# Performance work log

Hardware: AMD Instinct MI355X
Metric: run time of the kernel (lower is better)

Reference implementation:

```python
import math
import jax, jax.numpy as jnp
import numpy as np

B, N, M, C, H = 64, 64, 64, 512, 8
HD = C // H
FREQ = 256  # frequency_embedding_size
MAX_PERIOD = 10000.0


def setup_inputs() -> dict:
    key = jax.random.key(0)
    ks = jax.random.split(key, 10)
    s = 1.0 / math.sqrt(C)
    sf = 1.0 / math.sqrt(FREQ)
    return {
        "query": jax.random.normal(ks[0], (B, N, C), jnp.float32),
        "query_pos": jax.random.uniform(ks[1], (1, N, M), jnp.float32),
        # projection weights stored as [in, out]
        "Wq": jax.random.normal(ks[2], (C, C), jnp.float32) * s,
        "bq": jnp.zeros((C,), jnp.float32),
        "Wk": jax.random.normal(ks[3], (C, C), jnp.float32) * s,  # no bias
        "Wv": jax.random.normal(ks[4], (C, C), jnp.float32) * s,
        "bv": jnp.zeros((C,), jnp.float32),
        "Wo": jax.random.normal(ks[5], (C, C), jnp.float32) * s,
        "bo": jnp.zeros((C,), jnp.float32),
        # ScalarEmbedder MLP: Linear(FREQ->C), SiLU, Linear(C->C)
        "W1": jax.random.normal(ks[6], (FREQ, C), jnp.float32) * sf,
        "b1": jnp.zeros((C,), jnp.float32),
        "W2": jax.random.normal(ks[7], (C, C), jnp.float32) * s,
        "b2": jnp.zeros((C,), jnp.float32),
    }


def _freqs():
    half = FREQ // 2
    return jnp.exp(-math.log(MAX_PERIOD) * jnp.arange(half, dtype=jnp.float32) / half)


def reference(query, query_pos, Wq, bq, Wk, Wv, bv, Wo, bo, W1, b1, W2, b2):
    Bq, Nq, Cq = query.shape
    Mk = query_pos.shape[-1]
    # --- ScalarEmbedder on flattened pairwise positions: [N*M] -> [N*M, C]
    t = query_pos.reshape(-1)                       # [Bp*N*M], Bp = 1
    tf = t[:, None] * _freqs()[None, :]             # [N*M, FREQ/2]
    emb = jnp.concatenate([jnp.cos(tf), jnp.sin(tf)], axis=-1)  # [N*M, FREQ]
    pe = jax.nn.silu(emb @ W1 + b1) @ W2 + b2        # [N*M, C]
    pe = pe.reshape(Nq, Mk, H, HD).transpose(2, 0, 1, 3)  # [H, N, M, hd] (tiled over B via broadcast)

    q = (query @ Wq + bq).reshape(Bq, Nq, H, HD)     # bnhd
    k = (query @ Wk).reshape(Bq, Mk, H, HD)          # bmhd (key = query)
    v = (query @ Wv + bv).reshape(Bq, Mk, H, HD)

    scale = HD ** -0.5
    # attn[b,h,n,m] = sum_d q[b,n,h,d] * pe[h,n,m,d] * k[b,m,h,d]
    scores = jnp.einsum("bnhd,hnmd,bmhd->bhnm", q, pe, k) * scale
    attn = jax.nn.softmax(scores, axis=-1)
    x = jnp.einsum("bhnm,bmhd->bnhd", attn, v).reshape(Bq, Nq, Cq)
    return x @ Wo + bo + query  # identity = query
```

## Files before the change

kernel.cpp:

```cpp
#include <hip/hip_runtime.h>
#include <hip/hip_bf16.h>
#include <math.h>

typedef short short8 __attribute__((ext_vector_type(8)));
typedef float floatx4 __attribute__((ext_vector_type(4)));

__device__ __forceinline__ ushort f2bf(float f) {
    __hip_bfloat16 h = __float2bfloat16(f);
    return *reinterpret_cast<ushort*>(&h);
}
__device__ __forceinline__ void bf8_to_f32(uint4 u, float* f) {
    f[0] = __uint_as_float(u.x << 16); f[1] = __uint_as_float(u.x & 0xffff0000u);
    f[2] = __uint_as_float(u.y << 16); f[3] = __uint_as_float(u.y & 0xffff0000u);
    f[4] = __uint_as_float(u.z << 16); f[5] = __uint_as_float(u.z & 0xffff0000u);
    f[6] = __uint_as_float(u.w << 16); f[7] = __uint_as_float(u.w & 0xffff0000u);
}

#define GLDS16(g, l) __builtin_amdgcn_global_load_lds( \
    (const __attribute__((address_space(1))) void*)(g), \
    (__attribute__((address_space(3))) void*)(l), 16, 0, 0)

__global__ __launch_bounds__(256) void prep_kernel(
        const float* __restrict__ W1, const float* __restrict__ W2,
        const float* __restrict__ Wq, const float* __restrict__ Wk,
        const float* __restrict__ Wv, const float* __restrict__ Wo,
        const float* __restrict__ bq, const float* __restrict__ bv,
        const float* __restrict__ query, const float* __restrict__ qpos,
        ushort* __restrict__ W1t, ushort* __restrict__ W2t,
        ushort* __restrict__ Wqkvt, ushort* __restrict__ Wot,
        ushort* __restrict__ queryB, ushort* __restrict__ embB,
        float* __restrict__ biasC) {
    const int z = blockIdx.z;
    const int tx = threadIdx.x, ty = threadIdx.y;
    const int tid = ty * 32 + tx;
    if (z < 6) {
        const float* src; ushort* dst; int R;
        switch (z) {
            case 0:  src = W1; dst = W1t;              R = 256; break;
            case 1:  src = W2; dst = W2t;              R = 512; break;
            case 2:  src = Wq; dst = Wqkvt;            R = 512; break;
            case 3:  src = Wk; dst = Wqkvt + 512*512;  R = 512; break;
            case 4:  src = Wv; dst = Wqkvt + 1024*512; R = 512; break;
            default: src = Wo; dst = Wot;              R = 512; break;
        }
        const int r0 = blockIdx.y * 32, c0 = blockIdx.x * 32;
        if (r0 >= R) return;
        __shared__ float t[32][33];
        for (int i = ty; i < 32; i += 8) t[i][tx] = src[(size_t)(r0 + i) * 512 + c0 + tx];
        __syncthreads();
        for (int i = ty; i < 32; i += 8) dst[(size_t)(c0 + i) * R + r0 + tx] = f2bf(t[tx][i]);
    } else if (z == 6) {
        const int bid = blockIdx.y * 16 + blockIdx.x;
#pragma unroll
        for (int i = 0; i < 8; ++i) {
            size_t idx4 = (size_t)bid * 2048 + i * 256 + tid;
            float4 v = *(const float4*)(query + idx4 * 4);
            ushort4 o; o.x = f2bf(v.x); o.y = f2bf(v.y); o.z = f2bf(v.z); o.w = f2bf(v.w);
            *(ushort4*)(queryB + idx4 * 4) = o;
        }
        if (bid == 0) {
            for (int i = tid; i < 1536; i += 256)
                biasC[i] = (i < 512) ? bq[i] : ((i < 1024) ? 0.0f : bv[i - 1024]);
        }
    } else {
        const int bid = blockIdx.y * 16 + blockIdx.x;
        const int gt = bid * 256 + tid;
        const int e0 = gt * 16;
        const int r = e0 >> 8, j0 = e0 & 255;
        const float t = qpos[r];
        ushort o[16];
#pragma unroll
        for (int u = 0; u < 16; ++u) {
            int j = j0 + u, i = j & 127;
            float freq = __expf(-9.210340371976184f * (float)i * (1.0f / 128.0f));
            float a = t * freq;
            o[u] = f2bf((j < 128) ? __cosf(a) : __sinf(a));
        }
        *(uint4*)(embB + e0)     = *(uint4*)&o[0];
        *(uint4*)(embB + e0 + 8) = *(uint4*)&o[8];
    }
}

struct GArgs {
    const ushort* A; const ushort* Bt; const float* bias; const float* resid;
    void* C; int N, K, act, outf32, ntn;
};

template<int BM, int BN>
__global__ __launch_bounds__(256) void gemm_multi(GArgs g0, GArgs g1, int split) {
    constexpr int MR = BM / 32;
    constexpr int NR = BN / 32;
    __shared__ ushort As[2][BM * 32];
    __shared__ ushort Bs[2][BN * 32];

    const bool sel = ((int)blockIdx.x >= split);
    const GArgs g = sel ? g1 : g0;
    const int bid = sel ? ((int)blockIdx.x - split) : (int)blockIdx.x;
    const int tm = bid / g.ntn, tn = bid % g.ntn;
    const int row0 = tm * BM, col0 = tn * BN;
    const int K = g.K, N = g.N;

    const int tid = threadIdx.x;
    const int l = tid & 63, w = tid >> 6;
    const int wr = w >> 1, wc = w & 1;
    const int l15 = l & 15, quad = l >> 4;

    const int srow = tid >> 2;
    const int skoff = (tid & 3) * 8;
    const ushort* gA = g.A  + (size_t)(row0 + srow) * K + skoff;
    const ushort* gB = g.Bt + (size_t)(col0 + srow) * K + skoff;

    auto stage = [&](int s, int k0) {
#pragma unroll
        for (int i = 0; i < BM / 64; ++i)
            GLDS16(gA + (size_t)(i * 64) * K + k0, &As[s][(i * 256 + tid) * 8]);
#pragma unroll
        for (int i = 0; i < BN / 64; ++i)
            GLDS16(gB + (size_t)(i * 64) * K + k0, &Bs[s][(i * 256 + tid) * 8]);
    };

    floatx4 acc[MR][NR] = {};

    const int nk = K >> 5;
    stage(0, 0);
    int cur = 0;
    for (int t = 0; t < nk; ++t) {
        __syncthreads();
        if (t + 1 < nk) stage(cur ^ 1, (t + 1) * 32);
        short8 af[MR], bf[NR];
#pragma unroll
        for (int m = 0; m < MR; ++m)
            af[m] = *(const short8*)&As[cur][(wr * (BM / 2) + m * 16 + l15) * 32 + quad * 8];
#pragma unroll
        for (int n = 0; n < NR; ++n)
            bf[n] = *(const short8*)&Bs[cur][(wc * (BN / 2) + n * 16 + l15) * 32 + quad * 8];
#pragma unroll
        for (int m = 0; m < MR; ++m)
#pragma unroll
            for (int n = 0; n < NR; ++n)
                acc[m][n] = __builtin_amdgcn_mfma_f32_16x16x32_bf16(af[m], bf[n], acc[m][n], 0, 0, 0);
        cur ^= 1;
    }

#pragma unroll
    for (int m = 0; m < MR; ++m)
#pragma unroll
        for (int n = 0; n < NR; ++n) {
            int col = col0 + wc * (BN / 2) + n * 16 + l15;
            float bvv = g.bias ? g.bias[col] : 0.0f;
#pragma unroll
            for (int r = 0; r < 4; ++r) {
                int row = row0 + wr * (BM / 2) + m * 16 + quad * 4 + r;
                float val = acc[m][n][r] + bvv;
                if (g.act) val = val / (1.0f + __expf(-val));
                if (g.outf32) {
                    float rv = g.resid ? g.resid[(size_t)row * N + col] : 0.0f;
                    ((float*)g.C)[(size_t)row * N + col] = val + rv;
                } else {
                    ((ushort*)g.C)[(size_t)row * N + col] = f2bf(val);
                }
            }
        }
}

__global__ __launch_bounds__(256) void attn_bf16(
        const ushort* __restrict__ qkv, const ushort* __restrict__ peB,
        ushort* __restrict__ xB) {
    const int h = blockIdx.x, b = blockIdx.y, nh = blockIdx.z;
    const int tid = threadIdx.x;
    const int w = tid >> 6, l = tid & 63;
    const int lo = l & 7, hi = l >> 3;

    __shared__ float ks[64 * 64];
    __shared__ float vs[64 * 64];
    __shared__ float qs[32 * 64];

#pragma unroll
    for (int p = 0; p < 2; ++p) {
        int cid = p * 256 + tid;
        int row = cid >> 3, ch = cid & 7;
        const ushort* base = qkv + (size_t)(b * 64 + row) * 1536 + h * 64 + ch * 8;
        uint4 ku = *(const uint4*)(base + 512);
        uint4 vu = *(const uint4*)(base + 1024);
        float kf[8], vf[8];
        bf8_to_f32(ku, kf); bf8_to_f32(vu, vf);
#pragma unroll
        for (int j = 0; j < 8; ++j) {
            ks[row * 64 + ch * 8 + j] = kf[j];
            vs[row * 64 + ch * 8 + j] = vf[j];
        }
    }
    {
        int row = tid >> 3, ch = tid & 7;
        uint4 qu = *(const uint4*)(qkv + (size_t)(b * 64 + nh * 32 + row) * 1536 + h * 64 + ch * 8);
        float qf[8]; bf8_to_f32(qu, qf);
#pragma unroll
        for (int j = 0; j < 8; ++j) qs[row * 64 + ch * 8 + j] = qf[j];
    }
    __syncthreads();

    for (int i = 0; i < 8; ++i) {
        int nl = w + 4 * i;
        int n = nh * 32 + nl;
        float qf[8];
        *(float4*)&qf[0] = *(const float4*)&qs[nl * 64 + lo * 8];
        *(float4*)&qf[4] = *(const float4*)&qs[nl * 64 + lo * 8 + 4];

        float sreg[8];
#pragma unroll
        for (int mg = 0; mg < 8; ++mg) {
            int m = mg * 8 + hi;
            uint4 pu = *(const uint4*)(peB + (size_t)(n * 64 + m) * 512 + h * 64 + lo * 8);
            float pf[8]; bf8_to_f32(pu, pf);
            float kf[8];
            *(float4*)&kf[0] = *(const float4*)&ks[m * 64 + lo * 8];
            *(float4*)&kf[4] = *(const float4*)&ks[m * 64 + lo * 8 + 4];
            float p = 0.0f;
#pragma unroll
            for (int j = 0; j < 8; ++j) p = fmaf(qf[j] * kf[j], pf[j], p);
            p += __shfl_xor(p, 1);
            p += __shfl_xor(p, 2);
            p += __shfl_xor(p, 4);
            sreg[mg] = p * 0.125f;
        }

        float mx = sreg[0];
#pragma unroll
        for (int mg = 1; mg < 8; ++mg) mx = fmaxf(mx, sreg[mg]);
        mx = fmaxf(mx, __shfl_xor(mx, 8));
        mx = fmaxf(mx, __shfl_xor(mx, 16));
        mx = fmaxf(mx, __shfl_xor(mx, 32));
        float sum = 0.0f;
#pragma unroll
        for (int mg = 0; mg < 8; ++mg) { sreg[mg] = __expf(sreg[mg] - mx); sum += sreg[mg]; }
        sum += __shfl_xor(sum, 8);
        sum += __shfl_xor(sum, 16);
        sum += __shfl_xor(sum, 32);
        float rs = 1.0f / sum;

        float acc[8] = {};
#pragma unroll
        for (int mg = 0; mg < 8; ++mg) {
            int m = mg * 8 + hi;
            float at = sreg[mg] * rs;
            float vf[8];
            *(float4*)&vf[0] = *(const float4*)&vs[m * 64 + lo * 8];
            *(float4*)&vf[4] = *(const float4*)&vs[m * 64 + lo * 8 + 4];
#pragma unroll
            for (int j = 0; j < 8; ++j) acc[j] = fmaf(at, vf[j], acc[j]);
        }
#pragma unroll
        for (int j = 0; j < 8; ++j) {
            acc[j] += __shfl_xor(acc[j], 8);
            acc[j] += __shfl_xor(acc[j], 16);
            acc[j] += __shfl_xor(acc[j], 32);
        }
        if (l < 8) {
            uint4 o;
            o.x = f2bf(acc[0]) | ((uint)f2bf(acc[1]) << 16);
            o.y = f2bf(acc[2]) | ((uint)f2bf(acc[3]) << 16);
            o.z = f2bf(acc[4]) | ((uint)f2bf(acc[5]) << 16);
            o.w = f2bf(acc[6]) | ((uint)f2bf(acc[7]) << 16);
            *(uint4*)(xB + (size_t)(b * 64 + n) * 512 + h * 64 + l * 8) = o;
        }
    }
}

extern "C" void kernel_launch(void* const* d_in, const int* in_sizes, int n_in,
                              void* d_out, int out_size, void* d_ws, size_t ws_size,
                              hipStream_t stream) {
    const float* query = (const float*)d_in[0];
    const float* qpos  = (const float*)d_in[1];
    const float* Wq    = (const float*)d_in[2];
    const float* bq    = (const float*)d_in[3];
    const float* Wk    = (const float*)d_in[4];
    const float* Wv    = (const float*)d_in[5];
    const float* bv    = (const float*)d_in[6];
    const float* Wo    = (const float*)d_in[7];
    const float* bo    = (const float*)d_in[8];
    const float* W1    = (const float*)d_in[9];
    const float* b1    = (const float*)d_in[10];
    const float* W2    = (const float*)d_in[11];
    const float* b2    = (const float*)d_in[12];
    float* out = (float*)d_out;
    char* ws = (char*)d_ws;

    ushort* W1t    = (ushort*)(ws + 0);
    ushort* W2t    = (ushort*)(ws + 262144);
    ushort* Wqkvt  = (ushort*)(ws + 786432);
    ushort* Wot    = (ushort*)(ws + 2359296);
    float*  biasC  = (float*) (ws + 2883584);
    ushort* embB   = (ushort*)(ws + 3145728);
    ushort* queryB = (ushort*)(ws + 5242880);
    ushort* hiddenB= (ushort*)(ws + 9437184);
    ushort* peB    = (ushort*)(ws + 13631488);
    ushort* qkvB   = (ushort*)(ws + 17825792);
    ushort* xB     = (ushort*)(ws + 30408704);

    prep_kernel<<<dim3(16, 16, 8), dim3(32, 8), 0, stream>>>(
        W1, W2, Wq, Wk, Wv, Wo, bq, bv, query, qpos,
        W1t, W2t, Wqkvt, Wot, queryB, embB, biasC);

    GArgs a_g1 { embB,    W1t,   b1,    nullptr, hiddenB, 512,  256, 1, 0, 8  };
    GArgs a_g2 { hiddenB, W2t,   b2,    nullptr, peB,     512,  512, 0, 0, 8  };
    GArgs a_qkv{ queryB,  Wqkvt, biasC, nullptr, qkvB,    1536, 512, 0, 0, 24 };
    GArgs a_out{ xB,      Wot,   bo,    query,   out,     512,  512, 0, 1, 8  };

    gemm_multi<128, 64><<<256, 256, 0, stream>>>(a_g1, a_g1, 1 << 30);
    gemm_multi<128, 64><<<1024, 256, 0, stream>>>(a_g2, a_qkv, 256);

    attn_bf16<<<dim3(8, 64, 2), 256, 0, stream>>>(qkvB, peB, xB);

    gemm_multi<128, 64><<<256, 256, 0, stream>>>(a_out, a_out, 1 << 30);
}
```

Measured before the change: 171.2 us.

## Restructure attention PV stage via LDS probabilities, pad LDS, batch pe loads

The attention kernel now writes the normalized softmax probabilities (as bf16) into shared memory. A second phase has each thread compute a full 8-wide output chunk over all 64 keys, which removes the per-row cross-lane shuffle reductions and the lane-masked store. K/V shared arrays are padded to reduce bank conflicts. The eight pe loads per row are issued up front to raise memory-level parallelism. Q is read directly from global instead of being staged in LDS. The trade-off is an extra barrier, bf16 rounding of the attention weights, and higher register pressure from the prefetched pe vectors.

```diff
diff --git a/kernel.cpp b/kernel.cpp
--- a/kernel.cpp
+++ b/kernel.cpp
@@ -166,14 +166,16 @@
 __global__ __launch_bounds__(256) void attn_bf16(
         const ushort* __restrict__ qkv, const ushort* __restrict__ peB,
         ushort* __restrict__ xB) {
+    constexpr int LP = 68;
+    constexpr int PP = 66;
     const int h = blockIdx.x, b = blockIdx.y, nh = blockIdx.z;
     const int tid = threadIdx.x;
     const int w = tid >> 6, l = tid & 63;
     const int lo = l & 7, hi = l >> 3;
 
-    __shared__ float ks[64 * 64];
-    __shared__ float vs[64 * 64];
-    __shared__ float qs[32 * 64];
+    __shared__ float ks[64 * LP];
+    __shared__ float vs[64 * LP];
+    __shared__ ushort ps[32 * PP];
 
 #pragma unroll
     for (int p = 0; p < 2; ++p) {
@@ -186,35 +188,32 @@
         bf8_to_f32(ku, kf); bf8_to_f32(vu, vf);
 #pragma unroll
         for (int j = 0; j < 8; ++j) {
-            ks[row * 64 + ch * 8 + j] = kf[j];
-            vs[row * 64 + ch * 8 + j] = vf[j];
-        }
-    }
-    {
-        int row = tid >> 3, ch = tid & 7;
-        uint4 qu = *(const uint4*)(qkv + (size_t)(b * 64 + nh * 32 + row) * 1536 + h * 64 + ch * 8);
-        float qf[8]; bf8_to_f32(qu, qf);
-#pragma unroll
-        for (int j = 0; j < 8; ++j) qs[row * 64 + ch * 8 + j] = qf[j];
+            ks[row * LP + ch * 8 + j] = kf[j];
+            vs[row * LP + ch * 8 + j] = vf[j];
+        }
     }
     __syncthreads();
 
     for (int i = 0; i < 8; ++i) {
         int nl = w + 4 * i;
         int n = nh * 32 + nl;
-        float qf[8];
-        *(float4*)&qf[0] = *(const float4*)&qs[nl * 64 + lo * 8];
-        *(float4*)&qf[4] = *(const float4*)&qs[nl * 64 + lo * 8 + 4];
+
+        uint4 qu = *(const uint4*)(qkv + (size_t)(b * 64 + n) * 1536 + h * 64 + lo * 8);
+        float qf[8]; bf8_to_f32(qu, qf);
+
+        uint4 pu[8];
+#pragma unroll
+        for (int mg = 0; mg < 8; ++mg)
+            pu[mg] = *(const uint4*)(peB + (size_t)(n * 64 + mg * 8 + hi) * 512 + h * 64 + lo * 8);
 
         float sreg[8];
 #pragma unroll
         for (int mg = 0; mg < 8; ++mg) {
             int m = mg * 8 + hi;
-            uint4 pu = *(const uint4*)(peB + (size_t)(n * 64 + m) * 512 + h * 64 + lo * 8);
-            float pf[8]; bf8_to_f32(pu, pf);
+            float pf[8]; bf8_to_f32(pu[mg], pf);
             float kf[8];
-            *(float4*)&kf[0] = *(const float4*)&ks[m * 64 + lo * 8];
-            *(float4*)&kf[4] = *(const float4*)&ks[m * 64 + lo * 8 + 4];
+            *(float4*)&kf[0] = *(const float4*)&ks[m * LP + lo * 8];
+            *(float4*)&kf[4] = *(const float4*)&ks[m * LP + lo * 8 + 4];
             float p = 0.0f;
 #pragma unroll
             for (int j = 0; j < 8; ++j) p = fmaf(qf[j] * kf[j], pf[j], p);
@@ -238,31 +237,32 @@
         sum += __shfl_xor(sum, 32);
         float rs = 1.0f / sum;
 
+        float pv = sreg[0];
+#pragma unroll
+        for (int mg = 1; mg < 8; ++mg) if (lo == mg) pv = sreg[mg];
+        ps[nl * PP + 8 * lo + hi] = f2bf(pv * rs);
+    }
+    __syncthreads();
+
+    {
+        const int n8 = tid >> 3, dch = tid & 7;
         float acc[8] = {};
-#pragma unroll
-        for (int mg = 0; mg < 8; ++mg) {
-            int m = mg * 8 + hi;
-            float at = sreg[mg] * rs;
+#pragma unroll 4
+        for (int m = 0; m < 64; ++m) {
+            float at = __uint_as_float(((uint)ps[n8 * PP + m]) << 16);
             float vf[8];
-            *(float4*)&vf[0] = *(const float4*)&vs[m * 64 + lo * 8];
-            *(float4*)&vf[4] = *(const float4*)&vs[m * 64 + lo * 8 + 4];
+            *(float4*)&vf[0] = *(const float4*)&vs[m * LP + dch * 8];
+            *(float4*)&vf[4] = *(const float4*)&vs[m * LP + dch * 8 + 4];
 #pragma unroll
             for (int j = 0; j < 8; ++j) acc[j] = fmaf(at, vf[j], acc[j]);
         }
-#pragma unroll
-        for (int j = 0; j < 8; ++j) {
-            acc[j] += __shfl_xor(acc[j], 8);
-            acc[j] += __shfl_xor(acc[j], 16);
-            acc[j] += __shfl_xor(acc[j], 32);
-        }
-        if (l < 8) {
-            uint4 o;
-            o.x = f2bf(acc[0]) | ((uint)f2bf(acc[1]) << 16);
-            o.y = f2bf(acc[2]) | ((uint)f2bf(acc[3]) << 16);
-            o.z = f2bf(acc[4]) | ((uint)f2bf(acc[5]) << 16);
-            o.w = f2bf(acc[6]) | ((uint)f2bf(acc[7]) << 16);
-            *(uint4*)(xB + (size_t)(b * 64 + n) * 512 + h * 64 + l * 8) = o;
-        }
+        int n = nh * 32 + n8;
+        uint4 o;
+        o.x = f2bf(acc[0]) | ((uint)f2bf(acc[1]) << 16);
+        o.y = f2bf(acc[2]) | ((uint)f2bf(acc[3]) << 16);
+        o.z = f2bf(acc[4]) | ((uint)f2bf(acc[5]) << 16);
+        o.w = f2bf(acc[6]) | ((uint)f2bf(acc[7]) << 16);
+        *(uint4*)(xB + (size_t)(b * 64 + n) * 512 + h * 64 + dch * 8) = o;
     }
 }
 
```

Result: faster. 162.4 us (-5.1%).
